# Kernel tuning notes

Hardware: AMD Instinct MI355X
Metric: run time of the kernel (lower is better)

The kernel has to match this reference:

```python
import jax, jax.numpy as jnp
import numpy as np

# Dimensions
NT, NS = 1000, 2048   # timesteps, basins
NF, NG = 6, 32        # forcing channels, static attributes
NH, NR, HS = 16, 8, 256  # buckets, routing taps, hidden size
NK, NGD = 3, 9        # len(kDict)=3 (km,ki,ke), len(gDict)=9


def setup_inputs() -> dict:
    key = jax.random.key(0)
    ks = jax.random.split(key, 16)
    # Physically plausible forcings: Prcp/Evp nonnegative, T1<=T2 (min/max temp)
    Prcp = jax.random.uniform(ks[0], (NT, NS)) * 10.0
    Evp = jax.random.uniform(ks[1], (NT, NS)) * 5.0
    Tm = jax.random.normal(ks[2], (NT, NS)) * 10.0
    T1 = Tm - jax.random.uniform(ks[3], (NT, NS)) * 5.0
    T2 = Tm + jax.random.uniform(ks[4], (NT, NS)) * 5.0
    Rad = jax.random.uniform(ks[5], (NT, NS))
    Hum = jax.random.uniform(ks[6], (NT, NS))
    x = jnp.stack([Prcp, Evp, T1, T2, Rad, Hum], axis=-1)  # [nt, ns, 6]
    xc = jax.random.normal(ks[7], (NS, NG))

    def lin(k, fan_in, fan_out, s=0.05):
        k1, k2 = jax.random.split(k)
        return (jax.random.normal(k1, (fan_in, fan_out)) * s,
                jax.random.normal(k2, (fan_out,)) * s)

    W_fc, b_fc = lin(ks[8], NG, HS)
    W_r, b_r = lin(ks[9], HS, NH * (NR + 1))
    W_g, b_g = lin(ks[10], HS, NH * NGD)
    W_kin, b_kin = lin(ks[11], 4, HS)
    W_kout, b_kout = lin(ks[12], HS, NH * NK)
    return dict(x=x, xc=xc, W_fc=W_fc, b_fc=b_fc, W_r=W_r, b_r=b_r,
                W_g=W_g, b_g=b_g, W_kin=W_kin, b_kin=b_kin,
                W_kout=W_kout, b_kout=b_kout)


def _hardsigmoid(v):
    return jnp.clip(v / 6.0 + 0.5, 0.0, 1.0)


def _forward(x, xc, W_fc, b_fc, W_r, b_r, W_g, b_g, W_kin, b_kin, W_kout, b_kout):
    nt, ns, _ = x.shape
    Prcp, Evp, T1, T2 = x[..., 0], x[..., 1], x[..., 2], x[..., 3]
    f = x[..., 2:]                        # [nt, ns, 4] (T1,T2,Rad,Hum)

    # ---- getParam (eval mode: DropMask is identity) ----
    state = xc @ W_fc + b_fc              # [ns, hs]
    pK = jnp.tanh(f @ W_kin + b_kin + state) @ W_kout + b_kout  # [nt, ns, nh*3]
    hG = jnp.tanh(state)
    pG = hG @ W_g + b_g                   # [ns, nh*9]
    pR = hG @ W_r + b_r                   # [ns, nh*(nr+1)]

    # sepParam(K): km=exp, ki=relu, ke=exp  -> time-varying [nt, ns, nh]
    km = jnp.exp(pK[..., 0 * NH:1 * NH])
    ki = jax.nn.relu(pK[..., 1 * NH:2 * NH])
    ke = jnp.exp(pK[..., 2 * NH:3 * NH])

    # sepParam(G): static [ns, nh]
    g = lambda i: pG[..., i * NH:(i + 1) * NH]
    kp = jax.nn.sigmoid(g(0))
    ks_ = jax.nn.sigmoid(g(1))
    kd = jax.nn.sigmoid(g(2))
    gd = jax.nn.sigmoid(g(3))
    gl = (jax.nn.sigmoid(g(4)) * 10.0) ** 3
    qb = jax.nn.relu(g(5)) / 10.0
    ga = jax.nn.softmax(g(6), axis=-1)    # area weights over buckets
    gi = _hardsigmoid(g(7)) / 2.0
    ge = jax.nn.relu(g(8))

    # onePeakWeight: unimodal routing weights [ns, nh, nr]
    r = pR.reshape(ns, NH, NR + 1)
    s = jax.nn.softmax(r, axis=-1)
    c = jnp.cumsum(s, axis=-1)
    w = jnp.minimum(c, 1.0 - c + s)[..., :NR]
    wr = w / jnp.sum(w, axis=-1, keepdims=True)

    # divideP: snow/liquid split from min/max temperature crossing 0 C
    fl = jnp.clip(T2 / (T2 - T1 + 1e-5), 0.0, 1.0)  # liquid fraction
    Pl = (Prcp * fl)[..., None]           # [nt, ns, 1]
    Ps = (Prcp * (1.0 - fl))[..., None]
    Ev = Evp[..., None]

    # ---- bucket.step recurrence over time (the custom-scan hot loop) ----
    def step(carry, inp):
        Sf, Ss, Sg = carry                # each [ns, nh]
        Ps_t, Pl_t, Ev_t, km_t, ki_t, ke_t = inp
        # snow bucket: accumulate, melt capped by degree-day factor km
        Sf = Sf + Ps_t
        qf = jnp.minimum(Sf, km_t)
        Sf = Sf - qf
        # partition inflow: impervious/direct fraction gi
        inflow = qf + Pl_t
        qd = inflow * gi
        Ss = Ss + inflow * (1.0 - gi)
        # evapotranspiration
        E = jnp.minimum(jnp.maximum(Ss, 0.0), Ev_t * ke_t * ge)
        Ss = Ss - E
        # interflow capped by ki
        qi = jnp.minimum(ki_t, jnp.maximum(Ss, 0.0))
        Ss = Ss - qi
        # quick flow above capacity gl, slow drainage below
        qp = kp * jnp.maximum(Ss - gl, 0.0)
        qsa = ks_ * jnp.clip(Ss, 0.0, gl)
        Ss = Ss - qp - qsa
        # deep/groundwater bucket: fraction gd percolates, linear reservoir kd + baseflow qb
        Sg = Sg + qsa * gd
        qg = kd * Sg + qb
        Sg = Sg * (1.0 - kd)
        q = qp + qsa * (1.0 - gd) + qg + qd + qi
        return (Sf, Ss, Sg), q

    init = (jnp.zeros((ns, NH), x.dtype),
            jnp.zeros((ns, NH), x.dtype),
            jnp.zeros((ns, NH), x.dtype))
    _, Qp = jax.lax.scan(step, init, (Ps, Pl, Ev, km, ki, ke))  # [nt, ns, nh]

    # routing: valid temporal convolution with per-bucket unit hydrograph wr
    Tout = nt - NR + 1
    Q = jnp.zeros((Tout, ns, NH), Qp.dtype)
    for rr in range(NR):  # NR is a small fixed constant
        Q = Q + Qp[NR - 1 - rr: nt - rr] * wr[..., rr]
    yOut = jnp.sum(Q * ga, axis=-1)       # [Tout, ns]
    return yOut


def reference(x, xc, W_fc, b_fc, W_r, b_r, W_g, b_g, W_kin, b_kin, W_kout, b_kout):
    return _forward(x, xc, W_fc, b_fc, W_r, b_r, W_g, b_g, W_kin, b_kin, W_kout, b_kout)
```

## Files before the change

kernel.cpp:

```cpp
#include <hip/hip_runtime.h>
#include <hip/hip_bf16.h>

#define NT   1000
#define NS   2048
#define NH   16
#define NR   8
#define HS   256
#define TOUT 993

typedef __attribute__((ext_vector_type(8))) short short8;
typedef __attribute__((ext_vector_type(4))) float f32x4;

__device__ __forceinline__ ushort f2bf(float f) {
    union { float f; unsigned int u; } v; v.f = f;
    unsigned int u = v.u;
    return (ushort)((u + 0x7fffu + ((u >> 16) & 1u)) >> 16);
}
__device__ __forceinline__ float bf2f(ushort u) {
    union { unsigned int i; float f; } v; v.i = ((unsigned int)u) << 16; return v.f;
}
__device__ __forceinline__ unsigned int packbf2(float lo, float hi) {
    union { __hip_bfloat162 b; unsigned int u; } v;
    v.b = __float22bfloat162_rn(make_float2(lo, hi));
    return v.u;
}
__device__ __forceinline__ float sigf(float x) { return 1.f / (1.f + __expf(-x)); }
__device__ __forceinline__ float fast_tanh(float z) {
    float e = exp2f(z * 2.885390082f);
    return 1.f - 2.f * __builtin_amdgcn_rcpf(e + 1.f);
}
__device__ __forceinline__ float2 f2fma(float s, float2 w, float2 acc) {
    return make_float2(fmaf(s, w.x, acc.x), fmaf(s, w.y, acc.y));
}
template<int CTRL>
__device__ __forceinline__ float dpp_add(float v) {
    int s = __builtin_amdgcn_update_dpp(0, __builtin_bit_cast(int, v), CTRL, 0xf, 0xf, true);
    return v + __builtin_bit_cast(float, s);
}

__global__ __launch_bounds__(256) void kA(
    const float* __restrict__ xc, const float* __restrict__ W_fc, const float* __restrict__ b_fc,
    const float* __restrict__ W_r, const float* __restrict__ b_r,
    const float* __restrict__ W_g, const float* __restrict__ b_g,
    const float* __restrict__ b_kin, const float* __restrict__ W_kout,
    float* __restrict__ stateK, float* __restrict__ params, ushort* __restrict__ Wt_g)
{
    __shared__ float xcs[32];
    __shared__ float hG[256];
    __shared__ float pGR[288];
    const int s = blockIdx.x, tid = threadIdx.x;

    if (tid < 32) xcs[tid] = xc[s * 32 + tid];
    __syncthreads();

    float acc = b_fc[tid];
#pragma unroll 8
    for (int k = 0; k < 32; ++k) acc = fmaf(xcs[k], W_fc[k * 256 + tid], acc);
    stateK[s * 256 + tid] = acc + b_kin[tid];
    hG[tid] = tanhf(acc);
    __syncthreads();

    for (int j = tid; j < 288; j += 256) {
        const float* W = (j < 144) ? W_g : W_r;
        const float* b = (j < 144) ? b_g : b_r;
        int col = (j < 144) ? j : (j - 144);
        float a = b[col];
#pragma unroll 4
        for (int k = 0; k < 256; ++k) a = fmaf(hG[k], W[k * 144 + col], a);
        pGR[j] = a;
    }
    __syncthreads();

    if (tid < 16) {
        const int h = tid;
        float g0 = pGR[h],       g1 = pGR[16 + h],  g2 = pGR[32 + h];
        float g3 = pGR[48 + h],  g4 = pGR[64 + h],  g5 = pGR[80 + h];
        float g6 = pGR[96 + h],  g7 = pGR[112 + h], g8 = pGR[128 + h];
        float kp = sigf(g0), ksg = sigf(g1), kd = sigf(g2), gd = sigf(g3);
        float t4 = sigf(g4) * 10.f; float gl = t4 * t4 * t4;
        float qb = fmaxf(g5, 0.f) * 0.1f;
        float gi = fminf(fmaxf(g7 * (1.f / 6.f) + 0.5f, 0.f), 1.f) * 0.5f;
        float ge = fmaxf(g8, 0.f);
        float m = g6;
        for (int o = 1; o < 16; o <<= 1) m = fmaxf(m, __shfl_xor(m, o));
        float e = __expf(g6 - m), esum = e;
        for (int o = 1; o < 16; o <<= 1) esum += __shfl_xor(esum, o);
        float ga = e / esum;
        float r[9], rm = -1e30f;
#pragma unroll
        for (int i = 0; i < 9; ++i) { r[i] = pGR[144 + h * 9 + i]; rm = fmaxf(rm, r[i]); }
        float er[9], es = 0.f;
#pragma unroll
        for (int i = 0; i < 9; ++i) { er[i] = __expf(r[i] - rm); es += er[i]; }
        float inv_es = 1.f / es, c = 0.f, wsum = 0.f, w[8];
#pragma unroll
        for (int i = 0; i < 8; ++i) {
            float si = er[i] * inv_es; c += si;
            float wi = fminf(c, 1.f - c + si);
            w[i] = wi; wsum += wi;
        }
        const int base = s * 16 + h;
        params[0 * 32768 + base] = kp;  params[1 * 32768 + base] = ksg;
        params[2 * 32768 + base] = kd;  params[3 * 32768 + base] = gd;
        params[4 * 32768 + base] = gl;  params[5 * 32768 + base] = qb;
        params[6 * 32768 + base] = gi;  params[7 * 32768 + base] = ge;
        float sc = ga / wsum;
#pragma unroll
        for (int i = 0; i < 8; ++i) params[(8 + i) * 32768 + base] = w[i] * sc;
    }

    if (s == 0) {
        for (int i = tid; i < 48 * 256; i += 256) {
            int k = i / 48, col = i - k * 48;
            Wt_g[col * 264 + k] = f2bf(W_kout[i]);
        }
    }
}

__global__ __launch_bounds__(256, 3) void kB(
    const float* __restrict__ x,
    const float* __restrict__ stateK, const float* __restrict__ W_kin, const float* __restrict__ b_kout,
    const ushort* __restrict__ Wt_g,
    unsigned int* __restrict__ kmki, ushort* __restrict__ keA)
{
    __shared__ ushort Wt[48 * 264];
    __shared__ float  stS[16 * 260];
    __shared__ float  wkS[1024];
    const int tid = threadIdx.x;
    const int st = blockIdx.x & 127;
    const int tg = blockIdx.x >> 7;
    const int s0 = st << 4;

    for (int i = tid; i < 3168; i += 256)
        ((uint2*)Wt)[i] = ((const uint2*)Wt_g)[i];
#pragma unroll
    for (int i = tid; i < 1024; i += 256) {
        int row = i >> 6, c = (i & 63) << 2;
        *(float4*)(stS + row * 260 + c) = *(const float4*)(stateK + (s0 + row) * 256 + c);
    }
    *(float4*)(wkS + tid * 4) = ((const float4*)W_kin)[tid];
    __syncthreads();

    const int wv = tid >> 6, lane = tid & 63;
    const int mi = lane & 15, quad = lane >> 4;
    const int site = s0 + mi;
    const int t0 = tg * 20 + wv * 5;

    float xf[5][4];
#pragma unroll
    for (int ti = 0; ti < 5; ++ti) {
        const int xb = ((t0 + ti) * 2048 + site) * 6;
        float2 u23 = *(const float2*)(x + xb + 2);
        float2 u45 = *(const float2*)(x + xb + 4);
        xf[ti][0] = u23.x; xf[ti][1] = u23.y; xf[ti][2] = u45.x; xf[ti][3] = u45.y;
    }

    const float* stp = stS + mi * 260 + quad * 8;
    const float* wkp = wkS + quad * 8;
    const ushort* Wt0 = Wt + mi * 264 + quad * 8;

    f32x4 acc[5][3];
#pragma unroll
    for (int ti = 0; ti < 5; ++ti)
#pragma unroll
        for (int j = 0; j < 3; ++j) acc[ti][j] = (f32x4){0.f, 0.f, 0.f, 0.f};

#pragma unroll 1
    for (int kk = 0; kk < 8; ++kk) {
        const int ko = kk * 32;
        float4 sa  = *(const float4*)(stp + ko);
        float4 sb  = *(const float4*)(stp + ko + 4);
        float4 w0a = *(const float4*)(wkp + ko);
        float4 w0b = *(const float4*)(wkp + ko + 4);
        float4 w1a = *(const float4*)(wkp + 256 + ko);
        float4 w1b = *(const float4*)(wkp + 256 + ko + 4);
        float4 w2a = *(const float4*)(wkp + 512 + ko);
        float4 w2b = *(const float4*)(wkp + 512 + ko + 4);
        float4 w3a = *(const float4*)(wkp + 768 + ko);
        float4 w3b = *(const float4*)(wkp + 768 + ko + 4);
        short8 b0 = *(const short8*)(Wt0 + ko);
        short8 b1 = *(const short8*)(Wt0 + 16 * 264 + ko);
        short8 b2 = *(const short8*)(Wt0 + 32 * 264 + ko);
#pragma unroll
        for (int ti = 0; ti < 5; ++ti) {
            const float x0 = xf[ti][0], x1 = xf[ti][1], x2 = xf[ti][2], x3 = xf[ti][3];
            float2 z0 = make_float2(sa.x, sa.y), z1 = make_float2(sa.z, sa.w);
            float2 z2 = make_float2(sb.x, sb.y), z3 = make_float2(sb.z, sb.w);
            z0 = f2fma(x0, make_float2(w0a.x, w0a.y), z0);
            z1 = f2fma(x0, make_float2(w0a.z, w0a.w), z1);
            z2 = f2fma(x0, make_float2(w0b.x, w0b.y), z2);
            z3 = f2fma(x0, make_float2(w0b.z, w0b.w), z3);
            z0 = f2fma(x1, make_float2(w1a.x, w1a.y), z0);
            z1 = f2fma(x1, make_float2(w1a.z, w1a.w), z1);
            z2 = f2fma(x1, make_float2(w1b.x, w1b.y), z2);
            z3 = f2fma(x1, make_float2(w1b.z, w1b.w), z3);
            z0 = f2fma(x2, make_float2(w2a.x, w2a.y), z0);
            z1 = f2fma(x2, make_float2(w2a.z, w2a.w), z1);
            z2 = f2fma(x2, make_float2(w2b.x, w2b.y), z2);
            z3 = f2fma(x2, make_float2(w2b.z, w2b.w), z3);
            z0 = f2fma(x3, make_float2(w3a.x, w3a.y), z0);
            z1 = f2fma(x3, make_float2(w3a.z, w3a.w), z1);
            z2 = f2fma(x3, make_float2(w3b.x, w3b.y), z2);
            z3 = f2fma(x3, make_float2(w3b.z, w3b.w), z3);
            union { short8 s; unsigned int u[4]; } a;
            a.u[0] = packbf2(fast_tanh(z0.x), fast_tanh(z0.y));
            a.u[1] = packbf2(fast_tanh(z1.x), fast_tanh(z1.y));
            a.u[2] = packbf2(fast_tanh(z2.x), fast_tanh(z2.y));
            a.u[3] = packbf2(fast_tanh(z3.x), fast_tanh(z3.y));
            acc[ti][0] = __builtin_amdgcn_mfma_f32_16x16x32_bf16(a.s, b0, acc[ti][0], 0, 0, 0);
            acc[ti][1] = __builtin_amdgcn_mfma_f32_16x16x32_bf16(a.s, b1, acc[ti][1], 0, 0, 0);
            acc[ti][2] = __builtin_amdgcn_mfma_f32_16x16x32_bf16(a.s, b2, acc[ti][2], 0, 0, 0);
        }
    }

    const float bo0 = b_kout[mi], bo1 = b_kout[16 + mi], bo2 = b_kout[32 + mi];
#pragma unroll
    for (int ti = 0; ti < 5; ++ti) {
        const int t = t0 + ti;
#pragma unroll
        for (int reg = 0; reg < 4; ++reg) {
            float km = __expf(acc[ti][0][reg] + bo0);
            float ki = fmaxf(acc[ti][1][reg] + bo1, 0.f);
            float ke = __expf(acc[ti][2][reg] + bo2);
            const int idx = t * 32768 + (s0 + quad * 4 + reg) * 16 + mi;
            kmki[idx] = (unsigned int)f2bf(km) | ((unsigned int)f2bf(ki) << 16);
            keA[idx]  = f2bf(ke);
        }
    }
}

__global__ __launch_bounds__(64, 1) void kC(
    const float* __restrict__ x,
    const unsigned int* __restrict__ kmki, const ushort* __restrict__ keA,
    const float* __restrict__ params, float* __restrict__ yOut)
{
    const int gid = blockIdx.x * 64 + threadIdx.x;
    const int h = gid & 15, s = gid >> 4;

    const float kp  = params[0 * 32768 + gid];
    const float ksg = params[1 * 32768 + gid];
    const float kd  = params[2 * 32768 + gid];
    const float gd  = params[3 * 32768 + gid];
    const float gl  = params[4 * 32768 + gid];
    const float qbv = params[5 * 32768 + gid];
    const float gi  = params[6 * 32768 + gid];
    const float ge  = params[7 * 32768 + gid];
    float wrga[8];
#pragma unroll
    for (int i = 0; i < 8; ++i) wrga[i] = params[(8 + i) * 32768 + gid];

    float Sf = 0.f, Ss = 0.f, Sg = 0.f;
    float qh[8];
#pragma unroll
    for (int i = 0; i < 8; ++i) qh[i] = 0.f;

    unsigned int a0[8], a1[8]; ushort e0[8], e1[8];
    float2 ab0[8], cd0[8], ab1[8], cd1[8];

#define LOADB(B, tb) do {                                               \
        const int _b = (tb) * 8;                                        \
        _Pragma("unroll")                                               \
        for (int i = 0; i < 8; ++i) {                                   \
            a##B[i] = kmki[(_b + i) * 32768 + gid];                     \
            e##B[i] = keA[(_b + i) * 32768 + gid];                      \
            const int xb = ((_b + i) * 2048 + s) * 6;                   \
            ab##B[i] = *(const float2*)(x + xb);                        \
            cd##B[i] = *(const float2*)(x + xb + 2);                    \
        }                                                               \
    } while (0)

#define COMPUTEB(B, tb) do {                                            \
        float z[8];                                                     \
        _Pragma("unroll")                                               \
        for (int i = 0; i < 8; ++i) {                                   \
            float km = bf2f((ushort)(a##B[i] & 0xffffu));               \
            float ki = bf2f((ushort)(a##B[i] >> 16));                   \
            float ke = bf2f(e##B[i]);                                   \
            float Prcp = ab##B[i].x, ev = ab##B[i].y;                   \
            float T1 = cd##B[i].x, T2 = cd##B[i].y;                     \
            float fl = fminf(fmaxf(T2 * __builtin_amdgcn_rcpf(T2 - T1 + 1e-5f), 0.f), 1.f); \
            float pl = Prcp * fl;                                       \
            float ps = Prcp * (1.f - fl);                               \
            Sf += ps;                                                   \
            float qf = fminf(Sf, km); Sf -= qf;                         \
            float inflow = qf + pl;                                     \
            float qd = inflow * gi;                                     \
            Ss += inflow * (1.f - gi);                                  \
            float E = fminf(fmaxf(Ss, 0.f), ev * ke * ge); Ss -= E;     \
            float qi = fminf(ki, fmaxf(Ss, 0.f)); Ss -= qi;             \
            float qp = kp * fmaxf(Ss - gl, 0.f);                        \
            float qsa = ksg * fminf(fmaxf(Ss, 0.f), gl);                \
            Ss -= qp + qsa;                                             \
            Sg += qsa * gd;                                             \
            float qg = kd * Sg + qbv;                                   \
            Sg *= (1.f - kd);                                           \
            float q = qp + qsa * (1.f - gd) + qg + qd + qi;             \
            qh[i] = q;                                                  \
            float v = 0.f;                                              \
            _Pragma("unroll")                                           \
            for (int k = 0; k < 8; ++k) v = fmaf(wrga[k], qh[(i - k) & 7], v); \
            z[i] = v;                                                   \
        }                                                               \
        _Pragma("unroll")                                               \
        for (int i = 0; i < 8; ++i) z[i] = dpp_add<0xB1>(z[i]);    \
        _Pragma("unroll")                                               \
        for (int i = 0; i < 8; ++i) z[i] = dpp_add<0x4E>(z[i]);    \
        _Pragma("unroll")                                               \
        for (int i = 0; i < 8; ++i) z[i] = dpp_add<0x141>(z[i]);   \
        _Pragma("unroll")                                               \
        for (int i = 0; i < 8; ++i) z[i] = dpp_add<0x140>(z[i]);   \
        if (h == 0) {                                                   \
            const int tbase = (tb) * 8;                                 \
            _Pragma("unroll")                                           \
            for (int i = 0; i < 8; ++i) {                               \
                const int t = tbase + i;                                \
                if (t >= 7) yOut[(t - 7) * 2048 + s] = z[i];            \
            }                                                           \
        }                                                               \
    } while (0)

    LOADB(0, 0);
    LOADB(1, 1);

    for (int tb2 = 0; tb2 < 63; ++tb2) {
        const int tbA = 2 * tb2;
        COMPUTEB(0, tbA);
        {
            const int pf = (tbA + 2 < 125) ? tbA + 2 : 124;
            LOADB(0, pf);
        }
        const int tbB = 2 * tb2 + 1;
        if (tbB < 125) {
            COMPUTEB(1, tbB);
            const int pf = (tbB + 2 < 125) ? tbB + 2 : 124;
            LOADB(1, pf);
        }
    }
#undef LOADB
#undef COMPUTEB
}

extern "C" void kernel_launch(void* const* d_in, const int* in_sizes, int n_in,
                              void* d_out, int out_size, void* d_ws, size_t ws_size,
                              hipStream_t stream) {
    const float* x      = (const float*)d_in[0];
    const float* xc     = (const float*)d_in[1];
    const float* W_fc   = (const float*)d_in[2];
    const float* b_fc   = (const float*)d_in[3];
    const float* W_r    = (const float*)d_in[4];
    const float* b_r    = (const float*)d_in[5];
    const float* W_g    = (const float*)d_in[6];
    const float* b_g    = (const float*)d_in[7];
    const float* W_kin  = (const float*)d_in[8];
    const float* b_kin  = (const float*)d_in[9];
    const float* W_kout = (const float*)d_in[10];
    const float* b_kout = (const float*)d_in[11];
    float* yOut = (float*)d_out;

    char* ws = (char*)d_ws;
    float*  stateK = (float*)(ws + 0);
    float*  params = (float*)(ws + (2 << 20));
    ushort* Wt_g   = (ushort*)(ws + (4 << 20));
    unsigned int* kmki = (unsigned int*)(ws + (4 << 20) + (128 << 10));
    ushort* keA    = (ushort*)(kmki + (size_t)NT * NS * NH);

    hipLaunchKernelGGL(kA, dim3(2048), dim3(256), 0, stream,
                       xc, W_fc, b_fc, W_r, b_r, W_g, b_g, b_kin, W_kout,
                       stateK, params, Wt_g);
    hipLaunchKernelGGL(kB, dim3(128 * 50), dim3(256), 0, stream,
                       x, stateK, W_kin, b_kout, Wt_g, kmki, keA);
    hipLaunchKernelGGL(kC, dim3(512), dim3(64), 0, stream,
                       x, kmki, keA, params, yOut);
}
```

Baseline: 569.6 us.

## Precompute snow/rain split in kB and lay out scan inputs contiguously per site group

kB now computes the snow/liquid precipitation split and evaporation per site and time, and writes them to new buffers. Those buffers and the km/ki/ke arrays use a site-group-major layout, so each kC block (4 sites x 16 buckets) reads one contiguous chunk per timestep instead of gathering strided x rows across the whole basin dimension. The aim is to cut memory latency and improve coalescing in the serial, latency-bound scan kernel. The cost is extra global writes in kB and strided stores of kmki and keA there.

Measured after the change: 577.5 us. No clear change (+1.4%).

```diff
diff --git a/kernel.cpp b/kernel.cpp
--- a/kernel.cpp
+++ b/kernel.cpp
@@ -121,7 +121,8 @@
     const float* __restrict__ x,
     const float* __restrict__ stateK, const float* __restrict__ W_kin, const float* __restrict__ b_kout,
     const ushort* __restrict__ Wt_g,
-    unsigned int* __restrict__ kmki, ushort* __restrict__ keA)
+    unsigned int* __restrict__ kmki, ushort* __restrict__ keA,
+    float2* __restrict__ pspl, float* __restrict__ evA)
 {
     __shared__ ushort Wt[48 * 264];
     __shared__ float  stS[16 * 260];
@@ -149,10 +150,19 @@
     float xf[5][4];
 #pragma unroll
     for (int ti = 0; ti < 5; ++ti) {
-        const int xb = ((t0 + ti) * 2048 + site) * 6;
+        const int t = t0 + ti;
+        const int xb = (t * 2048 + site) * 6;
         float2 u23 = *(const float2*)(x + xb + 2);
         float2 u45 = *(const float2*)(x + xb + 4);
         xf[ti][0] = u23.x; xf[ti][1] = u23.y; xf[ti][2] = u45.x; xf[ti][3] = u45.y;
+        if (lane < 16) {
+            float2 u01 = *(const float2*)(x + xb);
+            float fl = fminf(fmaxf(u23.y * __builtin_amdgcn_rcpf(u23.y - u23.x + 1e-5f), 0.f), 1.f);
+            const int sg = st * 4 + (mi >> 2), sl = mi & 3;
+            const int mo = (sg * 1000 + t) * 4 + sl;
+            pspl[mo] = make_float2(u01.x * (1.f - fl), u01.x * fl);
+            evA[mo]  = u01.y;
+        }
     }
 
     const float* stp = stS + mi * 260 + quad * 8;
@@ -214,6 +224,7 @@
     }
 
     const float bo0 = b_kout[mi], bo1 = b_kout[16 + mi], bo2 = b_kout[32 + mi];
+    const int sgW = st * 4 + quad;
 #pragma unroll
     for (int ti = 0; ti < 5; ++ti) {
         const int t = t0 + ti;
@@ -222,7 +233,7 @@
             float km = __expf(acc[ti][0][reg] + bo0);
             float ki = fmaxf(acc[ti][1][reg] + bo1, 0.f);
             float ke = __expf(acc[ti][2][reg] + bo2);
-            const int idx = t * 32768 + (s0 + quad * 4 + reg) * 16 + mi;
+            const int idx = (sgW * 1000 + t) * 64 + (reg << 4) + mi;
             kmki[idx] = (unsigned int)f2bf(km) | ((unsigned int)f2bf(ki) << 16);
             keA[idx]  = f2bf(ke);
         }
@@ -230,12 +241,16 @@
 }
 
 __global__ __launch_bounds__(64, 1) void kC(
-    const float* __restrict__ x,
     const unsigned int* __restrict__ kmki, const ushort* __restrict__ keA,
+    const float2* __restrict__ pspl, const float* __restrict__ evA,
     const float* __restrict__ params, float* __restrict__ yOut)
 {
-    const int gid = blockIdx.x * 64 + threadIdx.x;
-    const int h = gid & 15, s = gid >> 4;
+    const int tid = threadIdx.x;
+    const int sg = blockIdx.x;
+    const int s = sg * 4 + (tid >> 4);
+    const int h = tid & 15;
+    const int gid = s * 16 + h;
+    const int sl = tid >> 4;
 
     const float kp  = params[0 * 32768 + gid];
     const float ksg = params[1 * 32768 + gid];
@@ -254,18 +269,19 @@
 #pragma unroll
     for (int i = 0; i < 8; ++i) qh[i] = 0.f;
 
+    const int base = sg * 1000;
+
     unsigned int a0[8], a1[8]; ushort e0[8], e1[8];
-    float2 ab0[8], cd0[8], ab1[8], cd1[8];
+    float2 p0[8], p1[8]; float v0[8], v1[8];
 
 #define LOADB(B, tb) do {                                               \
-        const int _b = (tb) * 8;                                        \
+        const int _b = base + (tb) * 8;                                 \
         _Pragma("unroll")                                               \
         for (int i = 0; i < 8; ++i) {                                   \
-            a##B[i] = kmki[(_b + i) * 32768 + gid];                     \
-            e##B[i] = keA[(_b + i) * 32768 + gid];                      \
-            const int xb = ((_b + i) * 2048 + s) * 6;                   \
-            ab##B[i] = *(const float2*)(x + xb);                        \
-            cd##B[i] = *(const float2*)(x + xb + 2);                    \
+            a##B[i] = kmki[(_b + i) * 64 + tid];                        \
+            e##B[i] = keA[(_b + i) * 64 + tid];                         \
+            p##B[i] = pspl[(_b + i) * 4 + sl];                          \
+            v##B[i] = evA[(_b + i) * 4 + sl];                           \
         }                                                               \
     } while (0)
 
@@ -276,11 +292,7 @@
             float km = bf2f((ushort)(a##B[i] & 0xffffu));               \
             float ki = bf2f((ushort)(a##B[i] >> 16));                   \
             float ke = bf2f(e##B[i]);                                   \
-            float Prcp = ab##B[i].x, ev = ab##B[i].y;                   \
-            float T1 = cd##B[i].x, T2 = cd##B[i].y;                     \
-            float fl = fminf(fmaxf(T2 * __builtin_amdgcn_rcpf(T2 - T1 + 1e-5f), 0.f), 1.f); \
-            float pl = Prcp * fl;                                       \
-            float ps = Prcp * (1.f - fl);                               \
+            float ps = p##B[i].x, pl = p##B[i].y, ev = v##B[i];         \
             Sf += ps;                                                   \
             float qf = fminf(Sf, km); Sf -= qf;                         \
             float inflow = qf + pl;                                     \
@@ -361,14 +373,17 @@
     float*  stateK = (float*)(ws + 0);
     float*  params = (float*)(ws + (2 << 20));
     ushort* Wt_g   = (ushort*)(ws + (4 << 20));
-    unsigned int* kmki = (unsigned int*)(ws + (4 << 20) + (128 << 10));
-    ushort* keA    = (ushort*)(kmki + (size_t)NT * NS * NH);
+    char*   p      = ws + (4 << 20) + (128 << 10);
+    float2* pspl   = (float2*)p;
+    float*  evA    = (float*)(p + 16384000);
+    unsigned int* kmki = (unsigned int*)(p + 16384000 + 8192000);
+    ushort* keA    = (ushort*)(p + 16384000 + 8192000 + 131072000);
 
     hipLaunchKernelGGL(kA, dim3(2048), dim3(256), 0, stream,
                        xc, W_fc, b_fc, W_r, b_r, W_g, b_g, b_kin, W_kout,
                        stateK, params, Wt_g);
     hipLaunchKernelGGL(kB, dim3(128 * 50), dim3(256), 0, stream,
-                       x, stateK, W_kin, b_kout, Wt_g, kmki, keA);
+                       x, stateK, W_kin, b_kout, Wt_g, kmki, keA, pspl, evA);
     hipLaunchKernelGGL(kC, dim3(512), dim3(64), 0, stream,
-                       x, kmki, keA, params, yOut);
-}
+                       kmki, keA, pspl, evA, params, yOut);
+}
```
